# Kernel optimization log

Measured on AMD Instinct MI355X. Metric: run time of the kernel, lower is better.

Reference implementation:

```python
import jax, jax.numpy as jnp
import numpy as np

D_MODEL = 2048
N_HEADS = 16
HEAD_DIM = D_MODEL // N_HEADS  # 128
ROPE_THETA = 10000.0
BATCH = 2
SEQ_LEN = 2048  # == window_size -> dense causal SDPA path


def setup_inputs() -> dict:
    key = jax.random.key(0)
    ks = jax.random.split(key, 5)
    scale = 1.0 / np.sqrt(D_MODEL)
    x = jax.random.normal(ks[0], (BATCH, SEQ_LEN, D_MODEL), dtype=jnp.float32)
    # torch nn.Linear weights are stored (out_features, in_features); y = x @ W.T
    Wq = jax.random.normal(ks[1], (D_MODEL, D_MODEL), dtype=jnp.float32) * scale
    Wk = jax.random.normal(ks[2], (D_MODEL, D_MODEL), dtype=jnp.float32) * scale
    Wv = jax.random.normal(ks[3], (D_MODEL, D_MODEL), dtype=jnp.float32) * scale
    Wo = jax.random.normal(ks[4], (D_MODEL, D_MODEL), dtype=jnp.float32) * scale
    return {"x": x, "Wq": Wq, "Wk": Wk, "Wv": Wv, "Wo": Wo}


def _apply_rope(x):
    # x: [B, H, S, HEAD_DIM]; interleaved-pair RoPE, positions 0..S-1
    S = x.shape[2]
    inv_freq = 1.0 / (ROPE_THETA ** (jnp.arange(0, HEAD_DIM, 2, dtype=jnp.float32) / HEAD_DIM))
    t = jnp.arange(S, dtype=jnp.float32)
    freqs = jnp.outer(t, inv_freq)            # [S, HEAD_DIM//2]
    cos = jnp.cos(freqs)
    sin = jnp.sin(freqs)
    x1 = x[..., 0::2]
    x2 = x[..., 1::2]
    rot = jnp.stack([x1 * cos - x2 * sin, x1 * sin + x2 * cos], axis=-1)  # [B,H,S,hd/2,2]
    return rot.reshape(x.shape)


def reference(x, Wq, Wk, Wv, Wo):
    B, S, _ = x.shape
    q = (x @ Wq.T).reshape(B, S, N_HEADS, HEAD_DIM).transpose(0, 2, 1, 3)  # [B,H,S,D]
    k = (x @ Wk.T).reshape(B, S, N_HEADS, HEAD_DIM).transpose(0, 2, 1, 3)
    v = (x @ Wv.T).reshape(B, S, N_HEADS, HEAD_DIM).transpose(0, 2, 1, 3)
    q = _apply_rope(q)
    k = _apply_rope(k)
    scores = jnp.einsum("bhqd,bhkd->bhqk", q, k) / np.sqrt(HEAD_DIM).astype(np.float32)
    causal = jnp.tril(jnp.ones((S, S), dtype=bool))
    scores = jnp.where(causal, scores, -jnp.inf)
    attn = jax.nn.softmax(scores, axis=-1)
    out = jnp.einsum("bhqk,bhkd->bhqd", attn, v)
    out = out.transpose(0, 2, 1, 3).reshape(B, S, N_HEADS * HEAD_DIM)
    return out @ Wo.T
```

## Files before the change

### kernel.cpp

```cpp
#include <hip/hip_runtime.h>
#include <stdint.h>

#define D_MODEL 2048
#define SEQ     2048
#define BATCH   2
#define NHEAD   16
#define HD      128
#define MROWS   (BATCH*SEQ)

typedef short short8 __attribute__((ext_vector_type(8)));
typedef float f32x4  __attribute__((ext_vector_type(4)));

__device__ __forceinline__ unsigned short f2b(float f) {
  unsigned int u = __float_as_uint(f);
  u += 0x7fffu + ((u >> 16) & 1u);
  return (unsigned short)(u >> 16);
}
__device__ __forceinline__ float b2f(unsigned short s) {
  return __uint_as_float(((unsigned int)s) << 16);
}
__device__ __forceinline__ void gll16(const void* g, void* l) {
  __builtin_amdgcn_global_load_lds((const __attribute__((address_space(1))) void*)g,
                                   (__attribute__((address_space(3))) void*)l, 16, 0, 0);
}
__device__ __forceinline__ void barrier_nodrain() {
  asm volatile("" ::: "memory");
  __builtin_amdgcn_s_barrier();
  asm volatile("" ::: "memory");
}
template<int N> __device__ __forceinline__ void vmwait() {
  if constexpr (N == 0)      asm volatile("s_waitcnt vmcnt(0)" ::: "memory");
  else if constexpr (N == 1) asm volatile("s_waitcnt vmcnt(1)" ::: "memory");
  else if constexpr (N == 2) asm volatile("s_waitcnt vmcnt(2)" ::: "memory");
  else if constexpr (N == 3) asm volatile("s_waitcnt vmcnt(3)" ::: "memory");
  else if constexpr (N == 4) asm volatile("s_waitcnt vmcnt(4)" ::: "memory");
  else if constexpr (N == 5) asm volatile("s_waitcnt vmcnt(5)" ::: "memory");
  else if constexpr (N == 6) asm volatile("s_waitcnt vmcnt(6)" ::: "memory");
  else if constexpr (N == 7) asm volatile("s_waitcnt vmcnt(7)" ::: "memory");
  else                       asm volatile("s_waitcnt vmcnt(8)" ::: "memory");
}

__global__ __launch_bounds__(256) void cast_all(
    const float* __restrict__ x,  const float* __restrict__ Wq,
    const float* __restrict__ Wk, const float* __restrict__ Wv,
    const float* __restrict__ Wo, unsigned short* __restrict__ dst)
{
  size_t e = ((size_t)blockIdx.x * 256 + threadIdx.x) * 4;
  const size_t XN = (size_t)MROWS * D_MODEL;
  const size_t WN = (size_t)D_MODEL * D_MODEL;
  const float* src; size_t off;
  if (e < XN) { src = x; off = e; }
  else {
    size_t e2 = e - XN;
    int w = (int)(e2 >> 22);
    off = e2 & (WN - 1);
    src = (w == 0) ? Wq : (w == 1) ? Wk : (w == 2) ? Wv : Wo;
  }
  float4 v = *(const float4*)(src + off);
  ushort4 o;
  o.x = f2b(v.x); o.y = f2b(v.y); o.z = f2b(v.z); o.w = f2b(v.w);
  *(ushort4*)(dst + e) = o;
}

template<int BM, int LA>
__device__ __forceinline__ void gemm_8ph(
    const unsigned short* __restrict__ A, const unsigned short* __restrict__ Bw,
    unsigned short* __restrict__ As, unsigned short* __restrict__ Bs,
    int m0, int n0, int tid, f32x4 (&acc)[BM / 32][4])
{
  constexpr int K = D_MODEL, NT = K / 64;
  constexpr int HA = BM / 2;
  constexpr int MI = BM / 32, MIH = MI / 2;
  constexpr int AHALF = HA * 64;
  constexpr int BHALF = 128 * 64;
  constexpr int P2N = 2 * (LA + 2);
  constexpr int P4N = 2 * LA + 2;
  const int wave = tid >> 6, lane = tid & 63, l15 = lane & 15, quad = lane >> 4;
  const int wr = wave >> 2, wc = wave & 3;
  const int rA = wr * 16 + l15;
  const int rB = wc * 16 + l15;
  const int swk = l15 & 7;

  auto stA = [&](int buf, int h, int t) {
    #pragma unroll
    for (int i = 0; i < LA; ++i) {
      int slot = i * 512 + tid, rw = slot >> 3, ch = slot & 7;
      gll16(A + (size_t)(m0 + h * HA + rw) * K + t * 64 + ((ch ^ (rw & 7)) * 8),
            As + (buf * 2 + h) * AHALF + (i * 512 + wave * 64) * 8);
    }
  };
  auto stB = [&](int buf, int h, int t) {
    #pragma unroll
    for (int i = 0; i < 2; ++i) {
      int slot = i * 512 + tid, rw = slot >> 3, ch = slot & 7;
      gll16(Bw + (size_t)(n0 + h * 128 + rw) * K + t * 64 + ((ch ^ (rw & 7)) * 8),
            Bs + (buf * 2 + h) * BHALF + (i * 512 + wave * 64) * 8);
    }
  };
  auto ldA = [&](int buf, int h, int ml, int ks) -> short8 {
    int rw = ml * 32 + rA;
    return *(const short8*)(As + (buf * 2 + h) * AHALF + rw * 64 + (((ks * 4 + quad) ^ swk) * 8));
  };
  auto ldB = [&](int buf, int h, int nl, int ks) -> short8 {
    int rw = nl * 64 + rB;
    return *(const short8*)(Bs + (buf * 2 + h) * BHALF + rw * 64 + (((ks * 4 + quad) ^ swk) * 8));
  };

  stA(0, 0, 0); stB(0, 0, 0); stA(0, 1, 0); stB(0, 1, 0);
  stA(1, 0, 1); stB(1, 1, 1);
  vmwait<LA + 2>();
  barrier_nodrain();

  short8 ah[MIH][2], b0[2][2], b1[2][2];

  #pragma unroll 1
  for (int t = 0; t < NT; ++t) {
    const int buf = t & 1;

    #pragma unroll
    for (int ml = 0; ml < MIH; ++ml) {
      ah[ml][0] = ldA(buf, 0, ml, 0); ah[ml][1] = ldA(buf, 0, ml, 1);
    }
    #pragma unroll
    for (int nl = 0; nl < 2; ++nl) {
      b0[nl][0] = ldB(buf, 0, nl, 0); b0[nl][1] = ldB(buf, 0, nl, 1);
    }
    if (t + 1 < NT) stB(buf ^ 1, 0, t + 1);
    barrier_nodrain();
    asm volatile("s_waitcnt lgkmcnt(0)" ::: "memory");
    __builtin_amdgcn_sched_barrier(0);
    __builtin_amdgcn_s_setprio(1);
    #pragma unroll
    for (int ml = 0; ml < MIH; ++ml)
      #pragma unroll
      for (int nl = 0; nl < 2; ++nl)
        #pragma unroll
        for (int ks = 0; ks < 2; ++ks)
          acc[ml][nl] = __builtin_amdgcn_mfma_f32_16x16x32_bf16(ah[ml][ks], b0[nl][ks], acc[ml][nl], 0, 0, 0);
    __builtin_amdgcn_s_setprio(0);
    barrier_nodrain();

    #pragma unroll
    for (int nl = 0; nl < 2; ++nl) {
      b1[nl][0] = ldB(buf, 1, nl, 0); b1[nl][1] = ldB(buf, 1, nl, 1);
    }
    if (t + 1 < NT) stA(buf ^ 1, 1, t + 1);
    if (t == NT - 1) vmwait<0>(); else vmwait<P2N>();
    barrier_nodrain();
    asm volatile("s_waitcnt lgkmcnt(0)" ::: "memory");
    __builtin_amdgcn_sched_barrier(0);
    __builtin_amdgcn_s_setprio(1);
    #pragma unroll
    for (int ml = 0; ml < MIH; ++ml)
      #pragma unroll
      for (int nl = 0; nl < 2; ++nl)
        #pragma unroll
        for (int ks = 0; ks < 2; ++ks)
          acc[ml][2 + nl] = __builtin_amdgcn_mfma_f32_16x16x32_bf16(ah[ml][ks], b1[nl][ks], acc[ml][2 + nl], 0, 0, 0);
    __builtin_amdgcn_s_setprio(0);
    barrier_nodrain();

    #pragma unroll
    for (int ml = 0; ml < MIH; ++ml) {
      ah[ml][0] = ldA(buf, 1, ml, 0); ah[ml][1] = ldA(buf, 1, ml, 1);
    }
    if (t + 2 < NT) stA(buf, 0, t + 2);
    barrier_nodrain();
    asm volatile("s_waitcnt lgkmcnt(0)" ::: "memory");
    __builtin_amdgcn_sched_barrier(0);
    __builtin_amdgcn_s_setprio(1);
    #pragma unroll
    for (int ml = 0; ml < MIH; ++ml)
      #pragma unroll
      for (int nl = 0; nl < 2; ++nl)
        #pragma unroll
        for (int ks = 0; ks < 2; ++ks)
          acc[MIH + ml][2 + nl] = __builtin_amdgcn_mfma_f32_16x16x32_bf16(ah[ml][ks], b1[nl][ks], acc[MIH + ml][2 + nl], 0, 0, 0);
    __builtin_amdgcn_s_setprio(0);
    barrier_nodrain();

    if (t + 2 < NT) stB(buf, 1, t + 2);
    if (t < NT - 1) { if (t == NT - 2) vmwait<LA>(); else vmwait<P4N>(); }
    barrier_nodrain();
    __builtin_amdgcn_s_setprio(1);
    #pragma unroll
    for (int ml = 0; ml < MIH; ++ml)
      #pragma unroll
      for (int nl = 0; nl < 2; ++nl)
        #pragma unroll
        for (int ks = 0; ks < 2; ++ks)
          acc[MIH + ml][nl] = __builtin_amdgcn_mfma_f32_16x16x32_bf16(ah[ml][ks], b0[nl][ks], acc[MIH + ml][nl], 0, 0, 0);
    __builtin_amdgcn_s_setprio(0);
    barrier_nodrain();
  }
}

__global__ __launch_bounds__(512, 2) void gemm_qkv3(
    const unsigned short* __restrict__ Axb, const unsigned short* __restrict__ Wqkv,
    unsigned short* __restrict__ Qh, unsigned short* __restrict__ Kh,
    unsigned short* __restrict__ Vt)
{
  __shared__ unsigned short As[2 * 2 * 128 * 64];
  __shared__ unsigned short Bs[2 * 2 * 128 * 64];
  const int m0 = blockIdx.y * 256, n0g = blockIdx.x * 256;
  f32x4 acc[8][4];
  #pragma unroll
  for (int i = 0; i < 8; ++i)
    #pragma unroll
    for (int j = 0; j < 4; ++j) acc[i][j] = (f32x4){0.f, 0.f, 0.f, 0.f};

  gemm_8ph<256, 2>(Axb, Wqkv, As, Bs, m0, n0g, threadIdx.x, acc);

  const int tid = threadIdx.x, wave = tid >> 6, lane = tid & 63;
  const int l15 = lane & 15, quad = lane >> 4, wr = wave >> 2, wc = wave & 3;
  const int z = n0g >> 11;
  if (z < 2) {
    unsigned short* dst = z ? Kh : Qh;
    #pragma unroll
    for (int mi = 0; mi < 8; ++mi)
      #pragma unroll
      for (int ni = 0; ni < 4; ++ni) {
        int row0 = m0 + mi * 32 + wr * 16 + quad * 4;
        int col  = (n0g + ni * 64 + wc * 16 + l15) & (D_MODEL - 1);
        int h = col >> 7, d = col & (HD - 1);
        #pragma unroll
        for (int r = 0; r < 4; ++r) {
          int m = row0 + r; int bb = m >> 11; int s = m & (SEQ - 1);
          dst[((size_t)(bb * NHEAD + h) * SEQ + s) * HD + d] = f2b(acc[mi][ni][r]);
        }
      }
  } else {
    #pragma unroll
    for (int mi = 0; mi < 8; ++mi)
      #pragma unroll
      for (int ni = 0; ni < 4; ++ni) {
        int row0 = m0 + mi * 32 + wr * 16 + quad * 4;
        int col  = (n0g + ni * 64 + wc * 16 + l15) & (D_MODEL - 1);
        int h = col >> 7, d = col & (HD - 1);
        int bb = row0 >> 11; int s = row0 & (SEQ - 1);
        ushort4 pk;
        pk.x = f2b(acc[mi][ni][0]); pk.y = f2b(acc[mi][ni][1]);
        pk.z = f2b(acc[mi][ni][2]); pk.w = f2b(acc[mi][ni][3]);
        *(ushort4*)(Vt + ((size_t)(bb * NHEAD + h) * HD + d) * SEQ + s) = pk;
      }
  }
}

__global__ __launch_bounds__(512, 2) void gemm_out3(
    const unsigned short* __restrict__ A, const unsigned short* __restrict__ Wo,
    float* __restrict__ C)
{
  __shared__ unsigned short As[2 * 2 * 64 * 64];
  __shared__ unsigned short Bs[2 * 2 * 128 * 64];
  const int m0 = blockIdx.y * 128, n0 = blockIdx.x * 256;
  f32x4 acc[4][4];
  #pragma unroll
  for (int i = 0; i < 4; ++i)
    #pragma unroll
    for (int j = 0; j < 4; ++j) acc[i][j] = (f32x4){0.f, 0.f, 0.f, 0.f};

  gemm_8ph<128, 1>(A, Wo, As, Bs, m0, n0, threadIdx.x, acc);

  const int tid = threadIdx.x, wave = tid >> 6, lane = tid & 63;
  const int l15 = lane & 15, quad = lane >> 4, wr = wave >> 2, wc = wave & 3;
  #pragma unroll
  for (int mi = 0; mi < 4; ++mi)
    #pragma unroll
    for (int ni = 0; ni < 4; ++ni) {
      int row0 = m0 + mi * 32 + wr * 16 + quad * 4;
      int col  = n0 + ni * 64 + wc * 16 + l15;
      #pragma unroll
      for (int r = 0; r < 4; ++r)
        C[(size_t)(row0 + r) * D_MODEL + col] = acc[mi][ni][r];
    }
}

__global__ __launch_bounds__(256) void rope_k(unsigned short* __restrict__ Qh,
                                              unsigned short* __restrict__ Kh)
{
  unsigned short* P = blockIdx.y ? Kh : Qh;
  int rid = blockIdx.x * 4 + (threadIdx.x >> 6);
  int i = threadIdx.x & 63;
  int s = rid & (SEQ - 1);
  size_t base = (size_t)rid * HD + 2 * i;
  float inv = exp2f(-(float)i * (13.287712379549449f / 64.0f));
  float ang = (float)s * inv;
  float sn, cs; sincosf(ang, &sn, &cs);
  unsigned int pk = *(const unsigned int*)(P + base);
  float x1 = b2f((unsigned short)(pk & 0xffffu));
  float x2 = b2f((unsigned short)(pk >> 16));
  unsigned short o0 = f2b(x1 * cs - x2 * sn);
  unsigned short o1 = f2b(x1 * sn + x2 * cs);
  *(unsigned int*)(P + base) = (unsigned int)o0 | ((unsigned int)o1 << 16);
}

__global__ __launch_bounds__(256) void attn_k(
    const unsigned short* __restrict__ Qh, const unsigned short* __restrict__ Kh,
    const unsigned short* __restrict__ Vt, unsigned short* __restrict__ Aout)
{
  __shared__ unsigned short Ks[64 * 128];
  __shared__ unsigned short Vs[128 * 64];
  __shared__ unsigned short sPb[4][16 * 72];
  const int tid = threadIdx.x;
  const int wave = tid >> 6, lane = tid & 63, l15 = lane & 15, quad = lane >> 4;
  const int bh = blockIdx.y;
  const int b = bh >> 4, h = bh & 15;
  const unsigned short* Qb = Qh + (size_t)bh * SEQ * HD;
  const unsigned short* Kb = Kh + (size_t)bh * SEQ * HD;
  const unsigned short* Vb = Vt + (size_t)bh * HD * SEQ;
  unsigned short* pw = &sPb[wave][0];
  const float scl = 0.08838834764831845f * 1.4426950408889634f;

  #pragma unroll
  for (int half = 0; half < 2; ++half) {
    const int tile = half ? (31 - blockIdx.x) : blockIdx.x;
    const int q0b = tile * 64;
    const int q0w = q0b + wave * 16;
    const int q = q0w + l15;

    short8 qf[4];
    #pragma unroll
    for (int c = 0; c < 4; ++c)
      qf[c] = *(const short8*)(Qb + (size_t)(q0w + l15) * HD + c * 32 + quad * 8);

    f32x4 o[8];
    #pragma unroll
    for (int dj = 0; dj < 8; ++dj) o[dj] = (f32x4){0.f, 0.f, 0.f, 0.f};
    float ms = -1e30f, ls = 0.f;

    const int trips = tile + 1;
    for (int it = 0; it < trips; ++it) {
      const int k0 = it * 64;
      __syncthreads();
      #pragma unroll
      for (int c = 0; c < 4; ++c) {
        int slot = c * 256 + tid;
        int kr = slot >> 4, pch = slot & 15;
        gll16(Kb + (size_t)(k0 + kr) * HD + ((pch ^ (kr & 15)) * 8), Ks + slot * 8);
      }
      #pragma unroll
      for (int c = 0; c < 4; ++c) {
        int slot = c * 256 + tid;
        int vr = slot >> 3, pch = slot & 7;
        gll16(Vb + (size_t)vr * SEQ + k0 + ((pch ^ (vr & 7)) * 8), Vs + slot * 8);
      }
      __syncthreads();

      f32x4 st[4];
      #pragma unroll
      for (int ni = 0; ni < 4; ++ni) st[ni] = (f32x4){0.f, 0.f, 0.f, 0.f};
      #pragma unroll
      for (int ni = 0; ni < 4; ++ni) {
        const int rowb = (ni * 16 + l15) * 128;
        #pragma unroll
        for (int c = 0; c < 4; ++c) {
          short8 kf = *(const short8*)(Ks + rowb + (((c * 4 + quad) ^ l15) * 8));
          st[ni] = __builtin_amdgcn_mfma_f32_16x16x32_bf16(kf, qf[c], st[ni], 0, 0, 0);
        }
      }

      if (k0 + 63 > q0w) {
        #pragma unroll
        for (int ni = 0; ni < 4; ++ni)
          #pragma unroll
          for (int r = 0; r < 4; ++r) {
            int k = k0 + ni * 16 + quad * 4 + r;
            if (k > q) st[ni][r] = -1e30f;
          }
      }

      float lm = -1e30f;
      #pragma unroll
      for (int ni = 0; ni < 4; ++ni)
        #pragma unroll
        for (int r = 0; r < 4; ++r) lm = fmaxf(lm, st[ni][r]);
      lm = fmaxf(lm, __shfl_xor(lm, 16, 64));
      lm = fmaxf(lm, __shfl_xor(lm, 32, 64));
      float mn = fmaxf(ms, lm);
      float al = exp2f((ms - mn) * scl);
      ms = mn;
      float nm = mn * scl;
      float rs = 0.f;
      #pragma unroll
      for (int ni = 0; ni < 4; ++ni)
        #pragma unroll
        for (int r = 0; r < 4; ++r) {
          float p = exp2f(fmaf(st[ni][r], scl, -nm));
          st[ni][r] = p;
          rs += p;
        }
      rs += __shfl_xor(rs, 16, 64);
      rs += __shfl_xor(rs, 32, 64);
      ls = ls * al + rs;
      #pragma unroll
      for (int dj = 0; dj < 8; ++dj) o[dj] *= al;

      #pragma unroll
      for (int ni = 0; ni < 4; ++ni) {
        ushort4 pk;
        pk.x = f2b(st[ni][0]); pk.y = f2b(st[ni][1]);
        pk.z = f2b(st[ni][2]); pk.w = f2b(st[ni][3]);
        *(ushort4*)(pw + l15 * 72 + ni * 16 + quad * 4) = pk;
      }
      short8 pf0 = *(const short8*)(pw + l15 * 72 + quad * 8);
      short8 pf1 = *(const short8*)(pw + l15 * 72 + 32 + quad * 8);

      #pragma unroll
      for (int dj = 0; dj < 8; ++dj) {
        const int vrow = (dj * 16 + l15) * 64;
        short8 v0 = *(const short8*)(Vs + vrow + (((quad) ^ (l15 & 7)) * 8));
        short8 v1 = *(const short8*)(Vs + vrow + (((4 + quad) ^ (l15 & 7)) * 8));
        o[dj] = __builtin_amdgcn_mfma_f32_16x16x32_bf16(v0, pf0, o[dj], 0, 0, 0);
        o[dj] = __builtin_amdgcn_mfma_f32_16x16x32_bf16(v1, pf1, o[dj], 0, 0, 0);
      }
    }

    float rl = 1.0f / ls;
    #pragma unroll
    for (int dj = 0; dj < 8; ++dj) {
      ushort4 pk;
      pk.x = f2b(o[dj][0] * rl); pk.y = f2b(o[dj][1] * rl);
      pk.z = f2b(o[dj][2] * rl); pk.w = f2b(o[dj][3] * rl);
      *(ushort4*)(Aout + ((size_t)(b * SEQ + q)) * D_MODEL + h * HD + dj * 16 + quad * 4) = pk;
    }
  }
}

extern "C" void kernel_launch(void* const* d_in, const int* in_sizes, int n_in,
                              void* d_out, int out_size, void* d_ws, size_t ws_size,
                              hipStream_t stream)
{
  const float* x  = (const float*)d_in[0];
  const float* Wq = (const float*)d_in[1];
  const float* Wk = (const float*)d_in[2];
  const float* Wv = (const float*)d_in[3];
  const float* Wo = (const float*)d_in[4];
  float* out = (float*)d_out;

  unsigned short* xb  = (unsigned short*)d_ws;
  unsigned short* wqb = xb  + 8388608;
  unsigned short* wkb = wqb + 4194304;
  unsigned short* wvb = wkb + 4194304;
  unsigned short* wob = wvb + 4194304;
  unsigned short* qh  = wob + 4194304;
  unsigned short* kh  = qh  + 8388608;
  unsigned short* vt  = kh  + 8388608;
  unsigned short* ao  = vt  + 8388608;

  (void)wkb; (void)wvb;
  cast_all<<<24576, 256, 0, stream>>>(x, Wq, Wk, Wv, Wo, xb);
  gemm_qkv3<<<dim3(24, 16), 512, 0, stream>>>(xb, wqb, qh, kh, vt);
  rope_k<<<dim3(16384, 2), 256, 0, stream>>>(qh, kh);
  attn_k<<<dim3(16, 32), 256, 0, stream>>>(qh, kh, vt, ao);
  gemm_out3<<<dim3(8, 32), 512, 0, stream>>>(ao, wob, out);
}
```

Baseline: 410.2 us.

## Double-buffer attention KV loads, add new pipelined out-proj GEMM, swizzle block order

The attention kernel now double-buffers K/V tiles in LDS, prefetching the next tile while computing the current one, and raises wave priority around its MFMA blocks. The output projection switches to a new gemm_pipe routine with a 128x256 tile and a different per-wave row/column mapping. Both GEMMs remap block indices so that consecutively scheduled blocks share operand tiles, which should improve L2 reuse. The double buffer doubles attention LDS use, which may lower occupancy, and the new GEMM's wait counts must match its load counts for correctness.

```diff
diff --git a/kernel.cpp b/kernel.cpp
--- a/kernel.cpp
+++ b/kernel.cpp
@@ -195,6 +195,121 @@
   }
 }
 
+template<int BM, int BN>
+__device__ __forceinline__ void gemm_pipe(
+    const unsigned short* __restrict__ A, const unsigned short* __restrict__ Bw,
+    unsigned short* __restrict__ As, unsigned short* __restrict__ Bs,
+    int m0, int n0, int tid, f32x4 (&acc)[BM / 32][4])
+{
+  constexpr int K  = D_MODEL;
+  constexpr int NT = K / 64;
+  constexpr int LA = BM / 64, LB = BN / 64;
+  constexpr int LT = LA + LB;
+  constexpr int MI = BM / 32, MH = MI / 2;
+  const int wave = tid >> 6, lane = tid & 63, l15 = lane & 15, quad = lane >> 4;
+  const int wr = wave >> 2, wc = wave & 3;
+  const int sw = l15 & 7;
+  const int arow = wr * (BM / 2) + l15;
+  const int brow = wc * (BN / 4) + l15;
+
+  auto stage = [&](int buf, int t) {
+    const int kt = t * 64;
+    #pragma unroll
+    for (int i = 0; i < LA; ++i) {
+      int slot = i * 512 + tid;
+      int row = slot >> 3, ch = slot & 7;
+      gll16(A + (size_t)(m0 + row) * K + kt + ((ch ^ (row & 7)) * 8),
+            As + (size_t)buf * (BM * 64) + (size_t)(i * 512 + wave * 64) * 8);
+    }
+    #pragma unroll
+    for (int i = 0; i < LB; ++i) {
+      int slot = i * 512 + tid;
+      int row = slot >> 3, ch = slot & 7;
+      gll16(Bw + (size_t)(n0 + row) * K + kt + ((ch ^ (row & 7)) * 8),
+            Bs + (size_t)buf * (BN * 64) + (size_t)(i * 512 + wave * 64) * 8);
+    }
+  };
+
+  stage(0, 0);
+  stage(1, 1);
+
+  short8 ah[MH][2], bf[4][2];
+
+  #pragma unroll 1
+  for (int t = 0; t < NT; ++t) {
+    const int cur = t & 1;
+    if (t < NT - 1) {
+      if constexpr (LT == 8) vmwait<8>(); else vmwait<6>();
+    } else {
+      vmwait<0>();
+    }
+    barrier_nodrain();
+
+    const unsigned short* as = As + cur * (BM * 64);
+    const unsigned short* bs = Bs + cur * (BN * 64);
+
+    #pragma unroll
+    for (int mi = 0; mi < MH; ++mi)
+      #pragma unroll
+      for (int ks = 0; ks < 2; ++ks)
+        ah[mi][ks] = *(const short8*)(as + (arow + mi * 16) * 64 + (((ks * 4 + quad) ^ sw) * 8));
+    #pragma unroll
+    for (int ni = 0; ni < 2; ++ni)
+      #pragma unroll
+      for (int ks = 0; ks < 2; ++ks)
+        bf[ni][ks] = *(const short8*)(bs + (brow + ni * 16) * 64 + (((ks * 4 + quad) ^ sw) * 8));
+    __builtin_amdgcn_s_setprio(1);
+    #pragma unroll
+    for (int mi = 0; mi < MH; ++mi)
+      #pragma unroll
+      for (int ni = 0; ni < 2; ++ni)
+        #pragma unroll
+        for (int ks = 0; ks < 2; ++ks)
+          acc[mi][ni] = __builtin_amdgcn_mfma_f32_16x16x32_bf16(ah[mi][ks], bf[ni][ks], acc[mi][ni], 0, 0, 0);
+    __builtin_amdgcn_s_setprio(0);
+
+    #pragma unroll
+    for (int ni = 2; ni < 4; ++ni)
+      #pragma unroll
+      for (int ks = 0; ks < 2; ++ks)
+        bf[ni][ks] = *(const short8*)(bs + (brow + ni * 16) * 64 + (((ks * 4 + quad) ^ sw) * 8));
+    __builtin_amdgcn_s_setprio(1);
+    #pragma unroll
+    for (int mi = 0; mi < MH; ++mi)
+      #pragma unroll
+      for (int ni = 2; ni < 4; ++ni)
+        #pragma unroll
+        for (int ks = 0; ks < 2; ++ks)
+          acc[mi][ni] = __builtin_amdgcn_mfma_f32_16x16x32_bf16(ah[mi][ks], bf[ni][ks], acc[mi][ni], 0, 0, 0);
+    __builtin_amdgcn_s_setprio(0);
+
+    #pragma unroll
+    for (int mi = 0; mi < MH; ++mi)
+      #pragma unroll
+      for (int ks = 0; ks < 2; ++ks)
+        ah[mi][ks] = *(const short8*)(as + (arow + (mi + MH) * 16) * 64 + (((ks * 4 + quad) ^ sw) * 8));
+    __builtin_amdgcn_s_setprio(1);
+    #pragma unroll
+    for (int mi = 0; mi < MH; ++mi)
+      #pragma unroll
+      for (int ni = 2; ni < 4; ++ni)
+        #pragma unroll
+        for (int ks = 0; ks < 2; ++ks)
+          acc[mi + MH][ni] = __builtin_amdgcn_mfma_f32_16x16x32_bf16(ah[mi][ks], bf[ni][ks], acc[mi + MH][ni], 0, 0, 0);
+    #pragma unroll
+    for (int mi = 0; mi < MH; ++mi)
+      #pragma unroll
+      for (int ni = 0; ni < 2; ++ni)
+        #pragma unroll
+        for (int ks = 0; ks < 2; ++ks)
+          acc[mi + MH][ni] = __builtin_amdgcn_mfma_f32_16x16x32_bf16(ah[mi][ks], bf[ni][ks], acc[mi + MH][ni], 0, 0, 0);
+    __builtin_amdgcn_s_setprio(0);
+
+    barrier_nodrain();
+    if (t + 2 < NT) stage(cur, t + 2);
+  }
+}
+
 __global__ __launch_bounds__(512, 2) void gemm_qkv3(
     const unsigned short* __restrict__ Axb, const unsigned short* __restrict__ Wqkv,
     unsigned short* __restrict__ Qh, unsigned short* __restrict__ Kh,
@@ -202,7 +317,10 @@
 {
   __shared__ unsigned short As[2 * 2 * 128 * 64];
   __shared__ unsigned short Bs[2 * 2 * 128 * 64];
-  const int m0 = blockIdx.y * 256, n0g = blockIdx.x * 256;
+  const int hw  = blockIdx.y * 24 + blockIdx.x;
+  const int swz = (hw & 7) * 48 + (hw >> 3);
+  const int m0  = (swz & 15) * 256;
+  const int n0g = (swz >> 4) * 256;
   f32x4 acc[8][4];
   #pragma unroll
   for (int i = 0; i < 8; ++i)
@@ -246,20 +364,23 @@
   }
 }
 
-__global__ __launch_bounds__(512, 2) void gemm_out3(
+__global__ __launch_bounds__(512, 2) void gemm_out2(
     const unsigned short* __restrict__ A, const unsigned short* __restrict__ Wo,
     float* __restrict__ C)
 {
-  __shared__ unsigned short As[2 * 2 * 64 * 64];
-  __shared__ unsigned short Bs[2 * 2 * 128 * 64];
-  const int m0 = blockIdx.y * 128, n0 = blockIdx.x * 256;
+  __shared__ unsigned short As[2 * 128 * 64];
+  __shared__ unsigned short Bs[2 * 256 * 64];
+  const int hw  = blockIdx.y * 8 + blockIdx.x;
+  const int swz = (hw & 7) * 32 + (hw >> 3);
+  const int m0  = (swz & 31) * 128;
+  const int n0  = (swz >> 5) * 256;
   f32x4 acc[4][4];
   #pragma unroll
   for (int i = 0; i < 4; ++i)
     #pragma unroll
     for (int j = 0; j < 4; ++j) acc[i][j] = (f32x4){0.f, 0.f, 0.f, 0.f};
 
-  gemm_8ph<128, 1>(A, Wo, As, Bs, m0, n0, threadIdx.x, acc);
+  gemm_pipe<128, 256>(A, Wo, As, Bs, m0, n0, threadIdx.x, acc);
 
   const int tid = threadIdx.x, wave = tid >> 6, lane = tid & 63;
   const int l15 = lane & 15, quad = lane >> 4, wr = wave >> 2, wc = wave & 3;
@@ -267,8 +388,8 @@
   for (int mi = 0; mi < 4; ++mi)
     #pragma unroll
     for (int ni = 0; ni < 4; ++ni) {
-      int row0 = m0 + mi * 32 + wr * 16 + quad * 4;
-      int col  = n0 + ni * 64 + wc * 16 + l15;
+      int row0 = m0 + wr * 64 + mi * 16 + quad * 4;
+      int col  = n0 + wc * 64 + ni * 16 + l15;
       #pragma unroll
       for (int r = 0; r < 4; ++r)
         C[(size_t)(row0 + r) * D_MODEL + col] = acc[mi][ni][r];
@@ -294,12 +415,12 @@
   *(unsigned int*)(P + base) = (unsigned int)o0 | ((unsigned int)o1 << 16);
 }
 
-__global__ __launch_bounds__(256) void attn_k(
+__global__ __launch_bounds__(256) void attn_k2(
     const unsigned short* __restrict__ Qh, const unsigned short* __restrict__ Kh,
     const unsigned short* __restrict__ Vt, unsigned short* __restrict__ Aout)
 {
-  __shared__ unsigned short Ks[64 * 128];
-  __shared__ unsigned short Vs[128 * 64];
+  __shared__ unsigned short Ks[2][64 * 128];
+  __shared__ unsigned short Vs[2][128 * 64];
   __shared__ unsigned short sPb[4][16 * 72];
   const int tid = threadIdx.x;
   const int wave = tid >> 6, lane = tid & 63, l15 = lane & 15, quad = lane >> 4;
@@ -311,11 +432,28 @@
   unsigned short* pw = &sPb[wave][0];
   const float scl = 0.08838834764831845f * 1.4426950408889634f;
 
+  auto stageKV = [&](int bsel, int it) {
+    const int k0 = it * 64;
+    unsigned short* kd = &Ks[bsel][0];
+    unsigned short* vd = &Vs[bsel][0];
+    #pragma unroll
+    for (int c = 0; c < 4; ++c) {
+      int slot = c * 256 + tid;
+      int kr = slot >> 4, pch = slot & 15;
+      gll16(Kb + (size_t)(k0 + kr) * HD + ((pch ^ (kr & 15)) * 8), kd + slot * 8);
+    }
+    #pragma unroll
+    for (int c = 0; c < 4; ++c) {
+      int slot = c * 256 + tid;
+      int vr = slot >> 3, pch = slot & 7;
+      gll16(Vb + (size_t)vr * SEQ + k0 + ((pch ^ (vr & 7)) * 8), vd + slot * 8);
+    }
+  };
+
   #pragma unroll
   for (int half = 0; half < 2; ++half) {
     const int tile = half ? (31 - blockIdx.x) : blockIdx.x;
-    const int q0b = tile * 64;
-    const int q0w = q0b + wave * 16;
+    const int q0w = tile * 64 + wave * 16;
     const int q = q0w + l15;
 
     short8 qf[4];
@@ -329,35 +467,31 @@
     float ms = -1e30f, ls = 0.f;
 
     const int trips = tile + 1;
+    stageKV(0, 0);
+    vmwait<0>(); barrier_nodrain();
+
     for (int it = 0; it < trips; ++it) {
+      const int cb = it & 1;
       const int k0 = it * 64;
-      __syncthreads();
-      #pragma unroll
-      for (int c = 0; c < 4; ++c) {
-        int slot = c * 256 + tid;
-        int kr = slot >> 4, pch = slot & 15;
-        gll16(Kb + (size_t)(k0 + kr) * HD + ((pch ^ (kr & 15)) * 8), Ks + slot * 8);
-      }
-      #pragma unroll
-      for (int c = 0; c < 4; ++c) {
-        int slot = c * 256 + tid;
-        int vr = slot >> 3, pch = slot & 7;
-        gll16(Vb + (size_t)vr * SEQ + k0 + ((pch ^ (vr & 7)) * 8), Vs + slot * 8);
-      }
-      __syncthreads();
+      if (it + 1 < trips) stageKV(cb ^ 1, it + 1);
+
+      const unsigned short* KsB = &Ks[cb][0];
+      const unsigned short* VsB = &Vs[cb][0];
 
       f32x4 st[4];
       #pragma unroll
       for (int ni = 0; ni < 4; ++ni) st[ni] = (f32x4){0.f, 0.f, 0.f, 0.f};
+      __builtin_amdgcn_s_setprio(1);
       #pragma unroll
       for (int ni = 0; ni < 4; ++ni) {
         const int rowb = (ni * 16 + l15) * 128;
         #pragma unroll
         for (int c = 0; c < 4; ++c) {
-          short8 kf = *(const short8*)(Ks + rowb + (((c * 4 + quad) ^ l15) * 8));
+          short8 kf = *(const short8*)(KsB + rowb + (((c * 4 + quad) ^ l15) * 8));
           st[ni] = __builtin_amdgcn_mfma_f32_16x16x32_bf16(kf, qf[c], st[ni], 0, 0, 0);
         }
       }
+      __builtin_amdgcn_s_setprio(0);
 
       if (k0 + 63 > q0w) {
         #pragma unroll
@@ -405,14 +539,19 @@
       short8 pf0 = *(const short8*)(pw + l15 * 72 + quad * 8);
       short8 pf1 = *(const short8*)(pw + l15 * 72 + 32 + quad * 8);
 
+      __builtin_amdgcn_s_setprio(1);
       #pragma unroll
       for (int dj = 0; dj < 8; ++dj) {
         const int vrow = (dj * 16 + l15) * 64;
-        short8 v0 = *(const short8*)(Vs + vrow + (((quad) ^ (l15 & 7)) * 8));
-        short8 v1 = *(const short8*)(Vs + vrow + (((4 + quad) ^ (l15 & 7)) * 8));
+        short8 v0 = *(const short8*)(VsB + vrow + (((quad) ^ (l15 & 7)) * 8));
+        short8 v1 = *(const short8*)(VsB + vrow + (((4 + quad) ^ (l15 & 7)) * 8));
         o[dj] = __builtin_amdgcn_mfma_f32_16x16x32_bf16(v0, pf0, o[dj], 0, 0, 0);
         o[dj] = __builtin_amdgcn_mfma_f32_16x16x32_bf16(v1, pf1, o[dj], 0, 0, 0);
       }
+      __builtin_amdgcn_s_setprio(0);
+
+      vmwait<0>();
+      barrier_nodrain();
     }
 
     float rl = 1.0f / ls;
@@ -451,6 +590,6 @@
   cast_all<<<24576, 256, 0, stream>>>(x, Wq, Wk, Wv, Wo, xb);
   gemm_qkv3<<<dim3(24, 16), 512, 0, stream>>>(xb, wqb, qh, kh, vt);
   rope_k<<<dim3(16384, 2), 256, 0, stream>>>(qh, kh);
-  attn_k<<<dim3(16, 32), 256, 0, stream>>>(qh, kh, vt, ao);
-  gemm_out3<<<dim3(8, 32), 512, 0, stream>>>(ao, wob, out);
-}
+  attn_k2<<<dim3(16, 32), 256, 0, stream>>>(qh, kh, vt, ao);
+  gemm_out2<<<dim3(8, 32), 512, 0, stream>>>(ao, wob, out);
+}
```

Result: no change. 407.4 us (-0.7%).
